# Kernel tuning notes

Measured on AMD Instinct MI355X. Metric: run time of the kernel, lower is better.

The kernel has to match this reference:

```python
import jax, jax.numpy as jnp
import numpy as np

N_CLUSTERS = 10

def _conv(x, w, b, stride):
    y = jax.lax.conv_general_dilated(x, w, stride, 'VALID', dimension_numbers=('NCHW', 'OIHW', 'NCHW'))
    return y + b[None, :, None, None]

def _forward(x, conv1_w, conv1_b, conv2_w, conv2_b, conv3_w, conv3_b,
             anc0_w, anc0_b, anc1_w, anc1_b, anc2_w, anc2_b, anc3_w, anc3_b,
             W1_w, W1_b, U_w, U_b, V_w, V_b, Wa_w, Wa_b,
             cluster_w, cluster_b, cls_w, cls_b):
    # backbone: three stride-2 valid convs
    h1 = _conv(x, conv1_w, conv1_b, (2, 2))
    h2 = _conv(h1, conv2_w, conv2_b, (2, 2))
    h3 = _conv(h2, conv3_w, conv3_b, (2, 2))  # [1,512,63,63]
    ancs = [_conv(h3, anc0_w, anc0_b, (1, 1)),
            _conv(h3, anc1_w, anc1_b, (1, 1)),
            _conv(h3, anc2_w, anc2_b, (1, 1)),
            _conv(h3, anc3_w, anc3_b, (1, 1))]
    ksizes = [(3, 3), (1, 1), (3, 1), (1, 3)]
    Hf, Wf = h3.shape[2], h3.shape[3]
    feats, coords = [], []
    # feat_organizer: flatten each anchor map to [Ha*Wa, 1024] and build normalized box coords
    for a, (kh, kw) in zip(ancs, ksizes):
        C, Ha, Wa = a.shape[1], a.shape[2], a.shape[3]
        feats.append(a[0].reshape(C, Ha * Wa).T)
        ys, xs = jnp.meshgrid(jnp.arange(Ha, dtype=jnp.float32), jnp.arange(Wa, dtype=jnp.float32), indexing='ij')
        cx = (xs.reshape(-1) + kw * 0.5) / Wf
        cy = (ys.reshape(-1) + kh * 0.5) / Hf
        bw = jnp.full((Ha * Wa,), kw / Wf, jnp.float32)
        bh = jnp.full((Ha * Wa,), kh / Hf, jnp.float32)
        coords.append(jnp.stack([cx, cy, bw, bh], axis=1))
    feat = jnp.concatenate(feats, 0)      # [N,1024]
    coords = jnp.concatenate(coords, 0)   # [N,4]
    # gated-attention MLP (AttentionHead)
    hmid = jax.nn.relu(feat @ W1_w.T + W1_b)              # [N,512]
    u = jax.nn.sigmoid(hmid @ U_w.T + U_b)                # [N,256]
    v = jnp.tanh(hmid @ V_w.T + V_b)                      # [N,256]
    att = jax.nn.sigmoid((u * v) @ Wa_w.T + Wa_b)[:, 0]   # [N]
    # cluster_features: rank anchors by attention, split into equal clusters,
    # attention-weighted segment reduce of features and box coords per cluster
    N = att.shape[0]
    rank = jnp.argsort(jnp.argsort(-att))
    cid = (rank * N_CLUSTERS) // N                         # [N] int cluster ids
    sw = jax.ops.segment_sum(att, cid, num_segments=N_CLUSTERS)                       # [nc]
    fc = jax.ops.segment_sum(hmid * att[:, None], cid, num_segments=N_CLUSTERS) / (sw[:, None] + 1e-8)   # [nc,512]
    pc = jax.ops.segment_sum(coords * att[:, None], cid, num_segments=N_CLUSTERS) / (sw[:, None] + 1e-8) # [nc,4]
    # ClusterAttention: conv with kernel (1,512) == per-cluster dot product, softmax over clusters
    scores = fc @ cluster_w + cluster_b                    # [nc]
    att_c = jax.nn.softmax(scores)
    # attention_pooling: attention-weighted sum of cluster features
    final = (att_c[:, None] * fc).sum(0, keepdims=True)    # [1,512]
    logits = final @ cls_w.T + cls_b
    return jax.nn.softmax(logits, axis=1), att_c.reshape(1, N_CLUSTERS, 1), pc

def setup_inputs() -> dict:
    key = jax.random.key(0)
    ks = jax.random.split(key, 30)
    def rn(k, shape, scale=0.02):
        return jax.random.normal(k, shape, jnp.float32) * scale
    d = {}
    d['x'] = jax.random.normal(ks[0], (1, 3, 512, 512), jnp.float32)
    d['conv1_w'] = rn(ks[1], (128, 3, 3, 3));    d['conv1_b'] = jnp.zeros((128,), jnp.float32)
    d['conv2_w'] = rn(ks[2], (256, 128, 3, 3));  d['conv2_b'] = jnp.zeros((256,), jnp.float32)
    d['conv3_w'] = rn(ks[3], (512, 256, 3, 3));  d['conv3_b'] = jnp.zeros((512,), jnp.float32)
    d['anc0_w'] = rn(ks[4], (1024, 512, 3, 3));  d['anc0_b'] = jnp.zeros((1024,), jnp.float32)
    d['anc1_w'] = rn(ks[5], (1024, 512, 1, 1));  d['anc1_b'] = jnp.zeros((1024,), jnp.float32)
    d['anc2_w'] = rn(ks[6], (1024, 512, 3, 1));  d['anc2_b'] = jnp.zeros((1024,), jnp.float32)
    d['anc3_w'] = rn(ks[7], (1024, 512, 1, 3));  d['anc3_b'] = jnp.zeros((1024,), jnp.float32)
    d['W1_w'] = rn(ks[8], (512, 1024));          d['W1_b'] = jnp.zeros((512,), jnp.float32)
    d['U_w'] = rn(ks[9], (256, 512));            d['U_b'] = jnp.zeros((256,), jnp.float32)
    d['V_w'] = rn(ks[10], (256, 512));           d['V_b'] = jnp.zeros((256,), jnp.float32)
    d['Wa_w'] = rn(ks[11], (1, 256));            d['Wa_b'] = jnp.zeros((1,), jnp.float32)
    d['cluster_w'] = rn(ks[12], (512,));         d['cluster_b'] = jnp.zeros((), jnp.float32)
    d['cls_w'] = rn(ks[13], (10, 512));          d['cls_b'] = jnp.zeros((10,), jnp.float32)
    return d

def reference(x, conv1_w, conv1_b, conv2_w, conv2_b, conv3_w, conv3_b,
              anc0_w, anc0_b, anc1_w, anc1_b, anc2_w, anc2_b, anc3_w, anc3_b,
              W1_w, W1_b, U_w, U_b, V_w, V_b, Wa_w, Wa_b,
              cluster_w, cluster_b, cls_w, cls_b):
    return _forward(x, conv1_w, conv1_b, conv2_w, conv2_b, conv3_w, conv3_b,
                    anc0_w, anc0_b, anc1_w, anc1_b, anc2_w, anc2_b, anc3_w, anc3_b,
                    W1_w, W1_b, U_w, U_b, V_w, V_b, Wa_w, Wa_b,
                    cluster_w, cluster_b, cls_w, cls_b)
```

## Files before the change

kernel.cpp:

```cpp
#include <hip/hip_runtime.h>
#include <math.h>


#define NTOT 15376
#define PHALF 2032128
typedef unsigned short u16;
typedef unsigned long long u64;
typedef __attribute__((ext_vector_type(8))) short bf16x8;
typedef __attribute__((ext_vector_type(4))) float f32x4;

static __device__ __forceinline__ u16 f2bf(float x) {
    union { float f; unsigned u; } v; v.f = x;
    unsigned r = v.u + 0x7FFF + ((v.u >> 16) & 1);
    return (u16)(r >> 16);
}
static __device__ __forceinline__ float bf2f(u16 h) {
    union { unsigned u; float f; } v; v.u = ((unsigned)h) << 16;
    return v.f;
}

static __device__ __forceinline__ void glds16(const void* g, void* l) {
    __builtin_amdgcn_global_load_lds(
        (const __attribute__((address_space(1))) void*)g,
        (__attribute__((address_space(3))) void*)l,
        16, 0, 0);
}

__global__ __launch_bounds__(256) void prep_all(
    const float* __restrict__ s0, const float* __restrict__ s1,
    const float* __restrict__ s2, const float* __restrict__ s3,
    const float* __restrict__ s4, const float* __restrict__ s5,
    const float* __restrict__ s6, const float* __restrict__ s7,
    const float* __restrict__ s8, u16* __restrict__ dst,
    u16* __restrict__ UVsep,
    const float* __restrict__ c1w, u16* __restrict__ Wc1pk,
    const float* __restrict__ x, u16* __restrict__ x_t,
    const float* __restrict__ W1w, const float* __restrict__ W1b,
    const float* __restrict__ b0, const float* __restrict__ b1,
    const float* __restrict__ b2, const float* __restrict__ b3,
    float* __restrict__ hb)
{
    int b = blockIdx.x, t = threadIdx.x;
    if (b < 41600) {
        long i = (long)b * 256 + t;
        if (i >= 10649600L) return;
        const long c1 = 4718592L, c2 = 5242880L, c3 = 6815744L, c4 = 8388608L,
                   c5 = 8912896L, c7 = 9175040L, c8 = 9469952L;
        if (i >= c5 && i < c7) {
            long loc = i - c5;
            int ic = (int)(loc % 512);
            long row = loc / 512;
            const float* src = (row & 1) ? s6 : s5;
            long j = row >> 1;
            UVsep[loc] = f2bf(src[j * 512 + ic]);
            return;
        }
        const float* src; long base; int IC, NT;
        if      (i < c1) { src = s0; base = 0;  IC = 512;  NT = 9; }
        else if (i < c2) { src = s1; base = c1; IC = 512;  NT = 1; }
        else if (i < c3) { src = s2; base = c2; IC = 512;  NT = 3; }
        else if (i < c4) { src = s3; base = c3; IC = 512;  NT = 3; }
        else if (i < c5) { src = s4; base = c4; IC = 1024; NT = 1; }
        else if (i < c8) { src = s7; base = c7; IC = 128;  NT = 9; }
        else             { src = s8; base = c8; IC = 256;  NT = 9; }
        long loc = i - base;
        int ic = (int)(loc % IC);
        long r = loc / IC;
        int tt = (int)(r % NT);
        long oc = r / NT;
        dst[i] = f2bf(src[(oc * IC + ic) * NT + tt]);
    } else if (b < 41632) {
        int j = (b - 41600) * 256 + t;
        if (j < 8192) {
            int oc = j >> 6, k = j & 63;
            Wc1pk[j] = (k < 27) ? f2bf(c1w[oc * 27 + k]) : (u16)0;
        }
    } else if (b < 41887) {
        int sp = (b - 41632) * 256 + t;
        if (sp < 65025) {
            int oy = sp / 255, ox = sp - oy * 255;
            const float* base = x + (long)oy * 2 * 512 + ox * 2;
            u64 pk[16];
#pragma unroll
            for (int q = 0; q < 16; ++q) pk[q] = 0;
#pragma unroll
            for (int ic = 0; ic < 3; ++ic)
#pragma unroll
                for (int ky = 0; ky < 3; ++ky)
#pragma unroll
                    for (int kx = 0; kx < 3; ++kx) {
                        int k = ic * 9 + ky * 3 + kx;
                        float v = base[ic * 262144 + ky * 512 + kx];
                        pk[k >> 2] |= (u64)f2bf(v) << ((k & 3) * 16);
                    }
            u64* drow = (u64*)(x_t + (long)sp * 64);
#pragma unroll
            for (int q = 0; q < 16; ++q) drow[q] = pk[q];
        }
    } else {
        int w = t >> 6, l = t & 63;
        int idx = (b - 41887) * 4 + w;
        int a = idx >> 9, m = idx & 511;
        const float* ab = (a == 0) ? b0 : (a == 1) ? b1 : (a == 2) ? b2 : b3;
        float s = 0.f;
        for (int j = l; j < 1024; j += 64)
            s = fmaf(W1w[(long)m * 1024 + j], ab[j], s);
#pragma unroll
        for (int d = 1; d < 64; d <<= 1) s += __shfl_xor(s, d, 64);
        if (l == 0) hb[idx] = s + W1b[m];
    }
}

__global__ __launch_bounds__(256) void transp_w(
    const u16* __restrict__ Wpk, u16* __restrict__ WpkT)
{
    __shared__ u16 tile[64][65];
    int bid = blockIdx.x;
    int ocb = bid & 15;
    int rt  = bid >> 4;
    int kbase, rowlen; long sbase;
    if      (rt < 72)  { kbase = 0;    sbase = 0L;       rowlen = 4608; }
    else if (rt < 80)  { kbase = 4608; sbase = 4718592L; rowlen = 512;  }
    else if (rt < 104) { kbase = 5120; sbase = 5242880L; rowlen = 1536; }
    else               { kbase = 6656; sbase = 6815744L; rowlen = 1536; }
    int kloc0 = rt * 64 - kbase;
    int t = threadIdx.x, q = t >> 6, ln = t & 63;
#pragma unroll
    for (int i = 0; i < 16; ++i) {
        int ocl = q * 16 + i;
        tile[ocl][ln] = Wpk[sbase + (long)(ocb * 64 + ocl) * rowlen + kloc0 + ln];
    }
    __syncthreads();
#pragma unroll
    for (int i = 0; i < 16; ++i) {
        int kl = q * 16 + i;
        WpkT[(long)(rt * 64 + kl) * 1024 + ocb * 64 + ln] = tile[ln][kl];
    }
}

__global__ __launch_bounds__(256) void combA(
    const float* __restrict__ P, const float* __restrict__ hb,
    u16* __restrict__ Hfeat)
{
    int row = blockIdx.x;
    int oy = row / 61, ox = row - oy * 61;
    long n = (long)(oy * 63 + ox) * 512;
    int c = threadIdx.x * 2;
    float2 p0 = *(const float2*)(P + n + c);
    float2 p1 = *(const float2*)(P + PHALF + n + c);
    float2 p2 = *(const float2*)(P + 2L * PHALF + n + c);
    float2 p3 = *(const float2*)(P + 3L * PHALF + n + c);
    float2 bv = *(const float2*)(hb + c);
    float sx = ((p0.x + p1.x) + (p2.x + p3.x)) + bv.x;
    float sy = ((p0.y + p1.y) + (p2.y + p3.y)) + bv.y;
    unsigned pk = (unsigned)f2bf(fmaxf(sx, 0.f))
                | ((unsigned)f2bf(fmaxf(sy, 0.f)) << 16);
    *(unsigned*)(Hfeat + (long)row * 512 + c) = pk;
}

__global__ __launch_bounds__(256) void comb3(
    const float* __restrict__ P, const float* __restrict__ bias,
    u16* __restrict__ h3T)
{
    int row = blockIdx.x;
    int trg = (row / 63) * 65 + row % 63;
    long n = (long)row * 512;
    int c = threadIdx.x * 2;
    float2 q0 = *(const float2*)(P + n + c);
    float2 q1 = *(const float2*)(P + PHALF + n + c);
    float2 b  = *(const float2*)(bias + c);
    unsigned pk = (unsigned)f2bf(q0.x + q1.x + b.x)
                | ((unsigned)f2bf(q0.y + q1.y + b.y) << 16);
    *(unsigned*)(h3T + (long)trg * 512 + c) = pk;
}

template<int CMODE, int EMODE, int TMODE>
__global__ __launch_bounds__(256) void gemm_bt(
    const u16* __restrict__ A, const u16* __restrict__ B,
    const float* __restrict__ bias0, const float* __restrict__ bias1,
    const float* __restrict__ bias2, const float* __restrict__ bias3,
    void* __restrict__ Cout, float* __restrict__ Pbuf,
    int M, int N, int RSB, int Ktot, int OH, int OW, int obase)
{
    __shared__ u16 As[4096];
    __shared__ u16 Bs[8192];
    const int tid = threadIdx.x, w = tid >> 6, l = tid & 63;
    const int wr = w >> 1, wc = w & 1;
    const int sl = l & 7, sh = l >> 3, sx = sl ^ sh;

    int n0, m0;
    bool TW3 = false;
    int part = -1;
    int tbase = 0;
    const float* bias = bias0;
    constexpr int ICL2 = (TMODE == 5) ? 1 : (TMODE == 6) ? 2 : (TMODE == 9) ? 0 : 3;
    constexpr int ICK  = 1 << ICL2;
    int ntaps;

    if (TMODE == 8) {
        int job = blockIdx.x >> 8, sub = blockIdx.x & 255;
        n0 = (sub & 31) * 128; m0 = (sub >> 5) * 64;
        int anc;
        if      (job == 0) { anc = 0; ntaps = 3; tbase = 0; part = 0; }
        else if (job == 1) { anc = 0; ntaps = 2; tbase = 3; part = 1; }
        else if (job == 2) { anc = 0; ntaps = 2; tbase = 5; part = 2; }
        else if (job == 3) { anc = 0; ntaps = 2; tbase = 7; part = 3; }
        else if (job == 4) { anc = 1; ntaps = 1; }
        else if (job == 5) { anc = 2; ntaps = 3; }
        else               { anc = 3; ntaps = 3; }
        TW3 = (anc == 0 || anc == 3);
        A += (anc == 0) ? 0 : (anc == 1) ? 4608 : (anc == 2) ? 5120 : 6656;
        obase = (anc == 0) ? 0 : (anc == 1) ? 3721 : (anc == 2) ? 7690 : 11533;
        OH = (anc == 0 || anc == 2) ? 61 : 63;
        OW = (anc == 0 || anc == 3) ? 61 : 63;
        bias = bias0 + anc * 512;
    } else if (TMODE == 6 && EMODE == 7) {
        int half = blockIdx.y >> 3;
        n0 = blockIdx.x * 128; m0 = (blockIdx.y & 7) * 64;
        ntaps = half ? 5 : 4; tbase = half * 4;
        Cout = (void*)((float*)Cout + (long)half * PHALF);
    } else {
        n0 = blockIdx.x * 128; m0 = blockIdx.y * 64;
        ntaps = Ktot >> ICL2;
    }
    const long RSA = (TMODE == 8) ? 8192 : (long)Ktot * 64;
    const long RSB2 = (long)RSB * 2;

    int offB[4], ldsOffB[4], ldsOffA[2];
    const char* aBase[2];
    const char* bBase[4];
#pragma unroll
    for (int j = 0; j < 4; ++j) {
        int r = w * 32 + j * 8 + sh;
        int gn = n0 + r;
        if (CMODE == 0)      { gn = min(gn, 3968);  offB[j] = (gn / 63) * 65 + (gn % 63); }
        else if (CMODE == 1) { offB[j] = min(gn, N - 1); }
        else if (CMODE == 2) { gn = min(gn, 16128); offB[j] = (gn / 127) * 510 + (gn % 127) * 2; }
        else                 { gn = min(gn, 3968);  offB[j] = (gn / 63) * 254 + (gn % 63) * 2; }
        ldsOffB[j] = r * 128;
        bBase[j] = (const char*)B + (long)offB[j] * RSB2 + sx * 16;
    }
#pragma unroll
    for (int j = 0; j < 2; ++j) {
        int r = w * 16 + j * 8 + sh;
        ldsOffA[j] = r * 128;
        aBase[j] = (const char*)A + (long)(m0 + r) * RSA * 2 + sx * 16;
    }

    f32x4 acc[2][4];
#pragma unroll
    for (int a = 0; a < 2; ++a)
#pragma unroll
        for (int b = 0; b < 4; ++b) acc[a][b] = (f32x4){0.f, 0.f, 0.f, 0.f};

    for (int t_ = 0; t_ < ntaps; ++t_) {
        int te = t_ + tbase;
        long tOffB;
        if (TMODE == 8) {
            int trow_;
            if (TW3) { int q_ = (te * 11) >> 5; trow_ = q_ * 65 + (te - q_ * 3); }
            else       trow_ = te * 65;
            tOffB = (long)trow_ * RSB2;
        } else if (TMODE == 4) {
            tOffB = (long)te * 1024;
        } else if (TMODE == 5) {
            int q_ = (te * 11) >> 5;
            tOffB = (long)(q_ * 255 + (te - q_ * 3)) * RSB2;
        } else if (TMODE == 6) {
            int q_ = (te * 11) >> 5;
            tOffB = (long)(q_ * 127 + (te - q_ * 3)) * RSB2;
        } else {
            tOffB = 0;
        }
        long aOff = (long)te * (ICK * 128);
#pragma unroll
        for (int kb = 0; kb < ICK; ++kb) {
#pragma unroll
            for (int j = 0; j < 2; ++j)
                glds16(aBase[j] + aOff + kb * 128, (char*)As + ldsOffA[j]);
#pragma unroll
            for (int j = 0; j < 4; ++j)
                glds16(bBase[j] + tOffB + kb * 128, (char*)Bs + ldsOffB[j]);
            __syncthreads();
#pragma unroll
            for (int kk = 0; kk < 2; ++kk) {
                bf16x8 af[2], bfr[4];
#pragma unroll
                for (int f = 0; f < 2; ++f) {
                    int rm = wr * 32 + f * 16 + (l & 15);
                    af[f] = *(const bf16x8*)((const char*)As + rm * 128 +
                               (((kk * 4 + (l >> 4)) ^ (rm & 7)) * 16));
                }
#pragma unroll
                for (int f = 0; f < 4; ++f) {
                    int rn = wc * 64 + f * 16 + (l & 15);
                    bfr[f] = *(const bf16x8*)((const char*)Bs + rn * 128 +
                               (((kk * 4 + (l >> 4)) ^ (rn & 7)) * 16));
                }
#pragma unroll
                for (int fm = 0; fm < 2; ++fm)
#pragma unroll
                    for (int fn = 0; fn < 4; ++fn)
                        acc[fm][fn] = __builtin_amdgcn_mfma_f32_16x16x32_bf16(
                            af[fm], bfr[fn], acc[fm][fn], 0, 0, 0);
            }
            __syncthreads();
        }
    }

#pragma unroll
    for (int fm = 0; fm < 2; ++fm) {
        int gmb = m0 + wr * 32 + fm * 16 + (l >> 4) * 4;
#pragma unroll
        for (int fn = 0; fn < 4; ++fn) {
            int gn = n0 + wc * 64 + fn * 16 + (l & 15);
            f32x4 v = acc[fm][fn];
            if (EMODE == 2) {
                if (gn < N) {
                    int j0 = gmb >> 1;
                    float u0 = 1.f / (1.f + expf(-(v.x + bias0[j0])));
                    float t0 = tanhf(v.y + bias1[j0]);
                    float u1 = 1.f / (1.f + expf(-(v.z + bias0[j0 + 1])));
                    float t1 = tanhf(v.w + bias1[j0 + 1]);
                    float2 o = { u0 * t0 * bias2[j0], u1 * t1 * bias2[j0 + 1] };
                    *(float2*)((float*)Cout + (long)gn * 256 + j0) = o;
                }
            } else if (EMODE == 4) {
                if (gn < N) {
                    float4 bv = *(const float4*)(bias + gmb);
                    u64 pk = (u64)f2bf(v.x + bv.x)
                           | ((u64)f2bf(v.y + bv.y) << 16)
                           | ((u64)f2bf(v.z + bv.z) << 32)
                           | ((u64)f2bf(v.w + bv.w) << 48);
                    *(u64*)((u16*)Cout + (long)gn * M + gmb) = pk;
                }
            } else if (EMODE == 5) {
                if (TMODE == 8 && part >= 0) {
                    if (gn < 3969) {
                        float4 o = { v.x, v.y, v.z, v.w };
                        *(float4*)(Pbuf + (long)part * PHALF + (long)gn * 512 + gmb) = o;
                    }
                } else if (gn < 3969) {
                    int oy = gn / 63, ox = gn - oy * 63;
                    if (oy < OH && ox < OW) {
                        int trg = obase + oy * OW + ox;
                        float4 bv = *(const float4*)(bias + gmb);
                        u64 pk = (u64)f2bf(fmaxf(v.x + bv.x, 0.f))
                               | ((u64)f2bf(fmaxf(v.y + bv.y, 0.f)) << 16)
                               | ((u64)f2bf(fmaxf(v.z + bv.z, 0.f)) << 32)
                               | ((u64)f2bf(fmaxf(v.w + bv.w, 0.f)) << 48);
                        *(u64*)((u16*)Cout + (long)trg * M + gmb) = pk;
                    }
                }
            } else if (EMODE == 6) {
                if (gn < N) {
                    u64 pk = (u64)f2bf(v.x)
                           | ((u64)f2bf(v.y) << 16)
                           | ((u64)f2bf(v.z) << 32)
                           | ((u64)f2bf(v.w) << 48);
                    *(u64*)((u16*)Cout + (long)gn * M + gmb) = pk;
                }
            } else {
                if (gn < 3969) {
                    float4 o = { v.x, v.y, v.z, v.w };
                    *(float4*)((float*)Cout + (long)gn * 512 + gmb) = o;
                }
            }
        }
    }
}

__global__ __launch_bounds__(256) void att_v3(
    const float* __restrict__ UVw, const float* __restrict__ Wab,
    float* __restrict__ att, int* __restrict__ rank, int N)
{
    int t = threadIdx.x, l = t & 63, r = t >> 6;
    int n = blockIdx.x * 4 + r;
    if (t < 4 && blockIdx.x * 4 + t < N) rank[blockIdx.x * 4 + t] = 0;
    if (n >= N) return;
    float4 p = *(const float4*)(UVw + (long)n * 256 + l * 4);
    float s = (p.x + p.y) + (p.z + p.w);
#pragma unroll
    for (int d = 1; d < 64; d <<= 1) s += __shfl_xor(s, d, 64);
    if (l == 0) att[n] = 1.f / (1.f + expf(-(s + Wab[0])));
}

__global__ __launch_bounds__(256) void rank_partial(
    const float* __restrict__ att, int* __restrict__ rank, int N)
{
    __shared__ float sa[1024];
    int n = blockIdx.x * 256 + threadIdx.x;
    int base = blockIdx.y * 1024;
    int cnt = min(1024, N - base);
    for (int t = threadIdx.x; t < cnt; t += 256) sa[t] = att[base + t];
    __syncthreads();
    if (n >= N) return;
    float a = att[n];
    int r = 0;
    for (int t = 0; t < cnt; ++t) {
        float aj = sa[t];
        int j = base + t;
        r += (int)(aj > a) | ((int)(aj == a) & (int)(j < n));
    }
    atomicAdd(&rank[n], r);
}

#define FC_NB 256
#define FC_ROWS 61
__device__ __forceinline__ void anchor_coords(int n, float& cx, float& cy,
                                              float& bw, float& bh)
{
    int kh, kw, Wa, loc;
    if (n < 3721)       { kh = 3; kw = 3; Wa = 61; loc = n; }
    else if (n < 7690)  { kh = 1; kw = 1; Wa = 63; loc = n - 3721; }
    else if (n < 11533) { kh = 3; kw = 1; Wa = 63; loc = n - 7690; }
    else                { kh = 1; kw = 3; Wa = 61; loc = n - 11533; }
    int iy = loc / Wa, ix = loc - iy * Wa;
    cx = (ix + kw * 0.5f) * (1.f / 63.f);
    cy = (iy + kh * 0.5f) * (1.f / 63.f);
    bw = kw * (1.f / 63.f);
    bh = kh * (1.f / 63.f);
}

__global__ __launch_bounds__(256) void tail_part(
    const u16* __restrict__ Hfeat, const float* __restrict__ att,
    const int* __restrict__ rank, float* __restrict__ fcp,
    float* __restrict__ prt, int N)
{
    __shared__ float red[4][50];
    int t = threadIdx.x;
    if (blockIdx.x < FC_NB) {
        int b = blockIdx.x;
        int l = t & 63, r = t >> 6;
        float acc[10][8];
#pragma unroll
        for (int k = 0; k < 10; ++k)
#pragma unroll
            for (int e = 0; e < 8; ++e) acc[k][e] = 0.f;
        int n0 = b * FC_ROWS;
        for (int it = 0; it < 16; ++it) {
            int nl = it * 4 + r;
            int n = n0 + nl;
            if (nl >= FC_ROWS || n >= N) break;
            float a = att[n];
            int c = (rank[n] * 10) / N;
            bf16x8 h8 = *(const bf16x8*)(Hfeat + (long)n * 512 + l * 8);
            float hf[8];
#pragma unroll
            for (int e = 0; e < 8; ++e) hf[e] = bf2f((u16)h8[e]);
#pragma unroll
            for (int k = 0; k < 10; ++k) {
                float sel = (c == k) ? a : 0.f;
#pragma unroll
                for (int e = 0; e < 8; ++e)
                    acc[k][e] = fmaf(sel, hf[e], acc[k][e]);
            }
        }
        float* dst = fcp + (long)b * 5120 + l * 8;
#pragma unroll
        for (int k = 0; k < 10; ++k)
#pragma unroll
            for (int e = 0; e < 8; ++e) dst[k * 512 + e] = acc[k][e];
    } else {
        int b = blockIdx.x - FC_NB;
        int n = b * 256 + t;
        int l = t & 63, w = t >> 6;
        float a = 0.f, cx = 0.f, cy = 0.f, bw = 0.f, bh = 0.f;
        int c = -1;
        if (n < N) {
            a = att[n]; c = (rank[n] * 10) / N;
            anchor_coords(n, cx, cy, bw, bh);
        }
#pragma unroll
        for (int k = 0; k < 10; ++k) {
            float sel = (c == k) ? a : 0.f;
            float v[5] = {sel, sel * cx, sel * cy, sel * bw, sel * bh};
#pragma unroll
            for (int d = 0; d < 5; ++d) {
                float x = v[d];
#pragma unroll
                for (int s = 1; s < 64; s <<= 1) x += __shfl_xor(x, s, 64);
                if (l == 0) red[w][k * 5 + d] = x;
            }
        }
        __syncthreads();
        if (t < 50) prt[b * 50 + t] = red[0][t] + red[1][t] + red[2][t] + red[3][t];
    }
}

__global__ __launch_bounds__(256) void fc_sum(
    const float* __restrict__ fcp, float* __restrict__ fc_raw)
{
    int i = blockIdx.x * 256 + threadIdx.x;
    if (i >= 5120) return;
    float s = 0.f;
    for (int b = 0; b < FC_NB; ++b) s += fcp[(long)b * 5120 + i];
    fc_raw[i] = s;
}

__global__ __launch_bounds__(512) void final_kernel(
    const float* __restrict__ fc_raw, const float* __restrict__ prt,
    const float* __restrict__ cluster_w, const float* __restrict__ cluster_b,
    const float* __restrict__ cls_w, const float* __restrict__ cls_b,
    float* __restrict__ out)
{
    __shared__ float red[512];
    __shared__ float swpc[50];
    int t = threadIdx.x;
    if (t < 50) {
        float s = 0.f;
        for (int b = 0; b < 61; ++b) s += prt[b * 50 + t];
        swpc[t] = s;
    }
    __syncthreads();
    float fcn[10];
#pragma unroll
    for (int k = 0; k < 10; ++k)
        fcn[k] = fc_raw[k * 512 + t] / (swpc[k * 5] + 1e-8f);
    float cw = cluster_w[t];
    float sc[10];
#pragma unroll
    for (int k = 0; k < 10; ++k) {
        red[t] = fcn[k] * cw;
        __syncthreads();
        for (int s = 256; s > 0; s >>= 1) {
            if (t < s) red[t] += red[t + s];
            __syncthreads();
        }
        sc[k] = red[0] + cluster_b[0];
        __syncthreads();
    }
    float mx = sc[0];
#pragma unroll
    for (int k = 1; k < 10; ++k) mx = fmaxf(mx, sc[k]);
    float se = 0.f;
#pragma unroll
    for (int k = 0; k < 10; ++k) { sc[k] = expf(sc[k] - mx); se += sc[k]; }
    float inv = 1.f / se;
#pragma unroll
    for (int k = 0; k < 10; ++k) sc[k] *= inv;
    float fm = 0.f;
#pragma unroll
    for (int k = 0; k < 10; ++k) fm = fmaf(sc[k], fcn[k], fm);
    float lg[10];
#pragma unroll
    for (int c = 0; c < 10; ++c) {
        red[t] = fm * cls_w[c * 512 + t];
        __syncthreads();
        for (int s = 256; s > 0; s >>= 1) {
            if (t < s) red[t] += red[t + s];
            __syncthreads();
        }
        lg[c] = red[0] + cls_b[c];
        __syncthreads();
    }
    float mx2 = lg[0];
#pragma unroll
    for (int c = 1; c < 10; ++c) mx2 = fmaxf(mx2, lg[c]);
    float se2 = 0.f;
#pragma unroll
    for (int c = 0; c < 10; ++c) { lg[c] = expf(lg[c] - mx2); se2 += lg[c]; }
    float inv2 = 1.f / se2;
    if (t < 10) out[t] = lg[t] * inv2;
    if (t >= 10 && t < 20) out[t] = sc[t - 10];
    if (t >= 20 && t < 60) {
        int i = t - 20;
        int k = i >> 2, d = i & 3;
        out[t] = swpc[k * 5 + 1 + d] / (swpc[k * 5] + 1e-8f);
    }
}

extern "C" void kernel_launch(void* const* d_in, const int* in_sizes, int n_in,
                              void* d_out, int out_size, void* d_ws, size_t ws_size,
                              hipStream_t stream)
{
    const float* x    = (const float*)d_in[0];
    const float* c1w  = (const float*)d_in[1];   const float* c1b = (const float*)d_in[2];
    const float* c2w  = (const float*)d_in[3];   const float* c2b = (const float*)d_in[4];
    const float* c3w  = (const float*)d_in[5];   const float* c3b = (const float*)d_in[6];
    const float* a0w  = (const float*)d_in[7];   const float* a0b = (const float*)d_in[8];
    const float* a1w  = (const float*)d_in[9];   const float* a1b = (const float*)d_in[10];
    const float* a2w  = (const float*)d_in[11];  const float* a2b = (const float*)d_in[12];
    const float* a3w  = (const float*)d_in[13];  const float* a3b = (const float*)d_in[14];
    const float* W1w  = (const float*)d_in[15];  const float* W1b = (const float*)d_in[16];
    const float* Uw   = (const float*)d_in[17];  const float* Ub  = (const float*)d_in[18];
    const float* Vw   = (const float*)d_in[19];  const float* Vb  = (const float*)d_in[20];
    const float* Waw  = (const float*)d_in[21];  const float* Wab = (const float*)d_in[22];
    const float* clw  = (const float*)d_in[23];  const float* clb = (const float*)d_in[24];
    const float* clsw = (const float*)d_in[25];  const float* clsb= (const float*)d_in[26];
    float* out = (float*)d_out;

    float* ws = (float*)d_ws;
    u16*   Hfeat= (u16*)ws;
    u16*   h1T  = (u16*)(ws + 3936256);
    u16*   h2T  = (u16*)(ws + 8097856);
    u16*   h3T  = (u16*)(ws + 10162368);
    float* UVw  = ws + 11243968;
    u16*   x_t  = (u16*)(ws + 11243968);
    u16*   Wpk  = (u16*)(ws + 15180224);
    float* P    = ws + 15180224;
    u16*   WpkT = (u16*)(ws + 20505024);
    u16*   WcAll= (u16*)(ws + 24699328);
    float* hb   = ws + 26796480;
    float* att  = ws + 26798528;
    int*   rank = (int*)(ws + 26813904);
    float* fcr  = ws + 26829280;
    float* fcp  = ws + 26834400;
    float* prt  = ws + 28145120;
    u16*   Wc1pk= (u16*)(ws + 28148224);
    u16*   UVpk = (u16*)(ws + 28152320);

    u16* W1pk  = Wpk + 8388608;
    u16* Wc2pk = Wpk + 9175040;
    u16* Wc3pk = Wpk + 9469952;

    dim3 blk(256);
    const float* nul = nullptr;
    float* fnul = nullptr;

    prep_all<<<dim3(42399), blk, 0, stream>>>(a0w, a1w, a2w, a3w, W1w, Uw, Vw,
                                              c2w, c3w, Wpk, UVpk, c1w, Wc1pk,
                                              x, x_t, W1w, W1b, a0b, a1b, a2b,
                                              a3b, hb);

    gemm_bt<1,4,9><<<dim3(509, 2), blk, 0, stream>>>(Wc1pk, x_t, c1b, nul, nul, nul, h1T, fnul, 128, 65025, 64, 1, 0, 0, 0);

    transp_w<<<dim3(2048), blk, 0, stream>>>(Wpk, WpkT);
    gemm_bt<1,6,4><<<dim3(4, 128), blk, 0, stream>>>(WpkT, W1pk, nul, nul, nul, nul, WcAll, fnul, 8192, 512, 1024, 16, 0, 0, 0);

    gemm_bt<2,4,5><<<dim3(127, 4), blk, 0, stream>>>(Wc2pk, h1T, c2b, nul, nul, nul, h2T, fnul, 256, 16129, 128, 18, 0, 0, 0);
    gemm_bt<3,7,6><<<dim3(32, 16), blk, 0, stream>>>(Wc3pk, h2T, nul, nul, nul, nul, P, fnul, 512, 3969, 256, 36, 0, 0, 0);
    comb3<<<dim3(3969), blk, 0, stream>>>(P, c3b, h3T);

    gemm_bt<0,5,8><<<dim3(1792), blk, 0, stream>>>(WcAll, h3T, hb, nul, nul, nul, Hfeat, P, 512, 3969, 512, 0, 0, 0, 0);
    combA<<<dim3(3721), blk, 0, stream>>>(P, hb, Hfeat);

    gemm_bt<1,2,1><<<dim3(121, 8), blk, 0, stream>>>(UVpk, Hfeat, Ub, Vb, Waw, nul, UVw, fnul, 512, NTOT, 512, 8, 0, 0, 0);

    att_v3<<<dim3(3844), blk, 0, stream>>>(UVw, Wab, att, rank, NTOT);
    rank_partial<<<dim3(61, 16), blk, 0, stream>>>(att, rank, NTOT);
    tail_part<<<dim3(FC_NB + 61), blk, 0, stream>>>(Hfeat, att, rank, fcp, prt, NTOT);
    fc_sum<<<dim3(20), blk, 0, stream>>>(fcp, fcr);
    final_kernel<<<dim3(1), dim3(512), 0, stream>>>(fcr, prt, clw, clb, clsw, clsb, out);
}
```

Measured before the change: 302.8 us.

## Fuse anchor weight packing into transpose kernel and coarsen anchor-0 tap split

The anchor conv weights are now converted from fp32 and transposed straight into the transposed bf16 layout in a single kernel. This drops the intermediate packed buffer write and its re-read by the separate transpose kernel. The anchor-0 GEMM job is split across taps into 2 partial sums instead of 4, so combA reads 2 partial buffers instead of 4 and fewer blocks are launched. The cost is less parallelism per tap-split job and strided fp32 gathers in the transpose tile load.

```diff
diff --git a/kernel.cpp b/kernel.cpp
--- a/kernel.cpp
+++ b/kernel.cpp
@@ -27,11 +27,9 @@
 }
 
 __global__ __launch_bounds__(256) void prep_all(
-    const float* __restrict__ s0, const float* __restrict__ s1,
-    const float* __restrict__ s2, const float* __restrict__ s3,
     const float* __restrict__ s4, const float* __restrict__ s5,
     const float* __restrict__ s6, const float* __restrict__ s7,
-    const float* __restrict__ s8, u16* __restrict__ dst,
+    const float* __restrict__ s8, u16* __restrict__ Wpk,
     u16* __restrict__ UVsep,
     const float* __restrict__ c1w, u16* __restrict__ Wc1pk,
     const float* __restrict__ x, u16* __restrict__ x_t,
@@ -41,42 +39,40 @@
     float* __restrict__ hb)
 {
     int b = blockIdx.x, t = threadIdx.x;
-    if (b < 41600) {
+    if (b < 8832) {
         long i = (long)b * 256 + t;
-        if (i >= 10649600L) return;
-        const long c1 = 4718592L, c2 = 5242880L, c3 = 6815744L, c4 = 8388608L,
-                   c5 = 8912896L, c7 = 9175040L, c8 = 9469952L;
-        if (i >= c5 && i < c7) {
-            long loc = i - c5;
+        if (i >= 2260992L) return;
+        if (i < 524288L) {
+            Wpk[8388608L + i] = f2bf(s4[i]);
+        } else if (i < 786432L) {
+            long loc = i - 524288L;
             int ic = (int)(loc % 512);
             long row = loc / 512;
             const float* src = (row & 1) ? s6 : s5;
-            long j = row >> 1;
-            UVsep[loc] = f2bf(src[j * 512 + ic]);
-            return;
-        }
-        const float* src; long base; int IC, NT;
-        if      (i < c1) { src = s0; base = 0;  IC = 512;  NT = 9; }
-        else if (i < c2) { src = s1; base = c1; IC = 512;  NT = 1; }
-        else if (i < c3) { src = s2; base = c2; IC = 512;  NT = 3; }
-        else if (i < c4) { src = s3; base = c3; IC = 512;  NT = 3; }
-        else if (i < c5) { src = s4; base = c4; IC = 1024; NT = 1; }
-        else if (i < c8) { src = s7; base = c7; IC = 128;  NT = 9; }
-        else             { src = s8; base = c8; IC = 256;  NT = 9; }
-        long loc = i - base;
-        int ic = (int)(loc % IC);
-        long r = loc / IC;
-        int tt = (int)(r % NT);
-        long oc = r / NT;
-        dst[i] = f2bf(src[(oc * IC + ic) * NT + tt]);
-    } else if (b < 41632) {
-        int j = (b - 41600) * 256 + t;
+            UVsep[loc] = f2bf(src[(row >> 1) * 512 + ic]);
+        } else if (i < 1081344L) {
+            long loc = i - 786432L;
+            int ic = (int)(loc % 128);
+            long r = loc / 128;
+            int tt = (int)(r % 9);
+            long oc = r / 9;
+            Wpk[9175040L + loc] = f2bf(s7[(oc * 128 + ic) * 9 + tt]);
+        } else {
+            long loc = i - 1081344L;
+            int ic = (int)(loc % 256);
+            long r = loc / 256;
+            int tt = (int)(r % 9);
+            long oc = r / 9;
+            Wpk[9469952L + loc] = f2bf(s8[(oc * 256 + ic) * 9 + tt]);
+        }
+    } else if (b < 8864) {
+        int j = (b - 8832) * 256 + t;
         if (j < 8192) {
             int oc = j >> 6, k = j & 63;
             Wc1pk[j] = (k < 27) ? f2bf(c1w[oc * 27 + k]) : (u16)0;
         }
-    } else if (b < 41887) {
-        int sp = (b - 41632) * 256 + t;
+    } else if (b < 9119) {
+        int sp = (b - 8864) * 256 + t;
         if (sp < 65025) {
             int oy = sp / 255, ox = sp - oy * 255;
             const float* base = x + (long)oy * 2 * 512 + ox * 2;
@@ -99,7 +95,7 @@
         }
     } else {
         int w = t >> 6, l = t & 63;
-        int idx = (b - 41887) * 4 + w;
+        int idx = (b - 9119) * 4 + w;
         int a = idx >> 9, m = idx & 511;
         const float* ab = (a == 0) ? b0 : (a == 1) ? b1 : (a == 2) ? b2 : b3;
         float s = 0.f;
@@ -111,24 +107,27 @@
     }
 }
 
-__global__ __launch_bounds__(256) void transp_w(
-    const u16* __restrict__ Wpk, u16* __restrict__ WpkT)
+__global__ __launch_bounds__(256) void packT_anchor(
+    const float* __restrict__ a0w, const float* __restrict__ a1w,
+    const float* __restrict__ a2w, const float* __restrict__ a3w,
+    u16* __restrict__ WpkT)
 {
     __shared__ u16 tile[64][65];
     int bid = blockIdx.x;
     int ocb = bid & 15;
     int rt  = bid >> 4;
-    int kbase, rowlen; long sbase;
-    if      (rt < 72)  { kbase = 0;    sbase = 0L;       rowlen = 4608; }
-    else if (rt < 80)  { kbase = 4608; sbase = 4718592L; rowlen = 512;  }
-    else if (rt < 104) { kbase = 5120; sbase = 5242880L; rowlen = 1536; }
-    else               { kbase = 6656; sbase = 6815744L; rowlen = 1536; }
+    const float* src; int kbase, NT;
+    if      (rt < 72)  { src = a0w; kbase = 0;    NT = 9; }
+    else if (rt < 80)  { src = a1w; kbase = 4608; NT = 1; }
+    else if (rt < 104) { src = a2w; kbase = 5120; NT = 3; }
+    else               { src = a3w; kbase = 6656; NT = 3; }
     int kloc0 = rt * 64 - kbase;
+    int tap = kloc0 >> 9, ic0 = kloc0 & 511;
     int t = threadIdx.x, q = t >> 6, ln = t & 63;
 #pragma unroll
     for (int i = 0; i < 16; ++i) {
         int ocl = q * 16 + i;
-        tile[ocl][ln] = Wpk[sbase + (long)(ocb * 64 + ocl) * rowlen + kloc0 + ln];
+        tile[ocl][ln] = f2bf(src[((long)(ocb * 64 + ocl) * 512 + ic0 + ln) * NT + tap]);
     }
     __syncthreads();
 #pragma unroll
@@ -148,11 +147,9 @@
     int c = threadIdx.x * 2;
     float2 p0 = *(const float2*)(P + n + c);
     float2 p1 = *(const float2*)(P + PHALF + n + c);
-    float2 p2 = *(const float2*)(P + 2L * PHALF + n + c);
-    float2 p3 = *(const float2*)(P + 3L * PHALF + n + c);
     float2 bv = *(const float2*)(hb + c);
-    float sx = ((p0.x + p1.x) + (p2.x + p3.x)) + bv.x;
-    float sy = ((p0.y + p1.y) + (p2.y + p3.y)) + bv.y;
+    float sx = (p0.x + p1.x) + bv.x;
+    float sy = (p0.y + p1.y) + bv.y;
     unsigned pk = (unsigned)f2bf(fmaxf(sx, 0.f))
                 | ((unsigned)f2bf(fmaxf(sy, 0.f)) << 16);
     *(unsigned*)(Hfeat + (long)row * 512 + c) = pk;
@@ -201,12 +198,10 @@
         int job = blockIdx.x >> 8, sub = blockIdx.x & 255;
         n0 = (sub & 31) * 128; m0 = (sub >> 5) * 64;
         int anc;
-        if      (job == 0) { anc = 0; ntaps = 3; tbase = 0; part = 0; }
-        else if (job == 1) { anc = 0; ntaps = 2; tbase = 3; part = 1; }
-        else if (job == 2) { anc = 0; ntaps = 2; tbase = 5; part = 2; }
-        else if (job == 3) { anc = 0; ntaps = 2; tbase = 7; part = 3; }
-        else if (job == 4) { anc = 1; ntaps = 1; }
-        else if (job == 5) { anc = 2; ntaps = 3; }
+        if      (job == 0) { anc = 0; ntaps = 4; tbase = 0; part = 0; }
+        else if (job == 1) { anc = 0; ntaps = 5; tbase = 4; part = 1; }
+        else if (job == 2) { anc = 1; ntaps = 1; }
+        else if (job == 3) { anc = 2; ntaps = 3; }
         else               { anc = 3; ntaps = 3; }
         TW3 = (anc == 0 || anc == 3);
         A += (anc == 0) ? 0 : (anc == 1) ? 4608 : (anc == 2) ? 5120 : 6656;
@@ -618,21 +613,20 @@
     const float* nul = nullptr;
     float* fnul = nullptr;
 
-    prep_all<<<dim3(42399), blk, 0, stream>>>(a0w, a1w, a2w, a3w, W1w, Uw, Vw,
-                                              c2w, c3w, Wpk, UVpk, c1w, Wc1pk,
-                                              x, x_t, W1w, W1b, a0b, a1b, a2b,
-                                              a3b, hb);
+    packT_anchor<<<dim3(2048), blk, 0, stream>>>(a0w, a1w, a2w, a3w, WpkT);
+    prep_all<<<dim3(9631), blk, 0, stream>>>(W1w, Uw, Vw, c2w, c3w, Wpk, UVpk,
+                                             c1w, Wc1pk, x, x_t, W1w, W1b,
+                                             a0b, a1b, a2b, a3b, hb);
 
     gemm_bt<1,4,9><<<dim3(509, 2), blk, 0, stream>>>(Wc1pk, x_t, c1b, nul, nul, nul, h1T, fnul, 128, 65025, 64, 1, 0, 0, 0);
 
-    transp_w<<<dim3(2048), blk, 0, stream>>>(Wpk, WpkT);
     gemm_bt<1,6,4><<<dim3(4, 128), blk, 0, stream>>>(WpkT, W1pk, nul, nul, nul, nul, WcAll, fnul, 8192, 512, 1024, 16, 0, 0, 0);
 
     gemm_bt<2,4,5><<<dim3(127, 4), blk, 0, stream>>>(Wc2pk, h1T, c2b, nul, nul, nul, h2T, fnul, 256, 16129, 128, 18, 0, 0, 0);
     gemm_bt<3,7,6><<<dim3(32, 16), blk, 0, stream>>>(Wc3pk, h2T, nul, nul, nul, nul, P, fnul, 512, 3969, 256, 36, 0, 0, 0);
     comb3<<<dim3(3969), blk, 0, stream>>>(P, c3b, h3T);
 
-    gemm_bt<0,5,8><<<dim3(1792), blk, 0, stream>>>(WcAll, h3T, hb, nul, nul, nul, Hfeat, P, 512, 3969, 512, 0, 0, 0, 0);
+    gemm_bt<0,5,8><<<dim3(1280), blk, 0, stream>>>(WcAll, h3T, hb, nul, nul, nul, Hfeat, P, 512, 3969, 512, 0, 0, 0, 0);
     combA<<<dim3(3721), blk, 0, stream>>>(P, hb, Hfeat);
 
     gemm_bt<1,2,1><<<dim3(121, 8), blk, 0, stream>>>(UVpk, Hfeat, Ub, Vb, Waw, nul, UVw, fnul, 512, NTOT, 512, 8, 0, 0, 0);
```

Measured after the change: 284.4 us. 6.1% less time.
